# Kernel optimization log

Hardware: AMD Instinct MI355X
Metric: run time of the kernel (lower is better)

The kernel has to match this reference:

```python
import jax, jax.numpy as jnp
import numpy as np

N = 100000
E = 1600000
IN_F = 128
OUT_F = 32
HEADS = 6
NEG_SLOPE = 0.2


def setup_inputs() -> dict:
    key = jax.random.key(0)
    k1, k2, k3, k4, k5 = jax.random.split(key, 5)
    x = jax.random.normal(k1, (N, IN_F), dtype=jnp.float32)
    edge_index = jax.random.randint(k2, (2, E), 0, N, dtype=jnp.int64)
    # GATConv params (PyG layout): shared linear for src/dst, per-head attention vectors, bias
    glorot = lambda k, shape: jax.random.normal(k, shape, dtype=jnp.float32) * np.sqrt(2.0 / (shape[0] + shape[-1]))
    W = glorot(k3, (IN_F, HEADS * OUT_F))          # lin.weight^T
    att_src = glorot(k4, (HEADS, OUT_F)) * 0.1     # [H, C]
    att_dst = glorot(k5, (HEADS, OUT_F)) * 0.1
    bias = jnp.zeros((OUT_F,), dtype=jnp.float32)  # concat=False -> bias of size out_feature
    return {"x": x, "edge_index": edge_index, "W": W,
            "att_src": att_src, "att_dst": att_dst, "bias": bias}


def reference(x, edge_index, W, att_src, att_dst, bias):
    src, dst = edge_index[0], edge_index[1]
    # Linear projection to per-head features: [N, H, C]
    xp = (x @ W).reshape(N, HEADS, OUT_F)
    # Per-node attention logit halves: [N, H]
    a_s = jnp.einsum("nhc,hc->nh", xp, att_src)
    a_d = jnp.einsum("nhc,hc->nh", xp, att_dst)
    # Per-edge logits with LeakyReLU: [E, H]
    e = jax.nn.leaky_relu(a_s[src] + a_d[dst], negative_slope=NEG_SLOPE)
    # Segment softmax over edges grouped by destination node
    m = jax.ops.segment_max(e, dst, num_segments=N)            # [N, H]
    m = jnp.where(jnp.isfinite(m), m, 0.0)                     # empty segments -> -inf guard
    e = jnp.exp(e - m[dst])
    s = jax.ops.segment_sum(e, dst, num_segments=N)            # [N, H]
    alpha = e / (s[dst] + 1e-16)                               # [E, H]
    # Weighted scatter-add aggregation: [N, H, C]
    msg = xp[src] * alpha[:, :, None]
    out = jax.ops.segment_sum(msg, dst, num_segments=N)
    # concat=False -> mean over heads, add bias, then SELU
    out = out.mean(axis=1) + bias
    return jax.nn.selu(out)
```

## Files before the change

### kernel.cpp

```cpp
#include <hip/hip_runtime.h>


typedef __attribute__((ext_vector_type(8))) short short8;
typedef __attribute__((ext_vector_type(4))) float f32x4;

#define SK 136

__device__ __forceinline__ unsigned short f2bf(float f)
{
    unsigned int u = __float_as_uint(f);
    u = (u + 0x7fffu + ((u >> 16) & 1u)) >> 16;
    return (unsigned short)u;
}

__global__ __launch_bounds__(256) void k_prep(
    const float* __restrict__ W,
    const float* __restrict__ att_src, const float* __restrict__ att_dst,
    unsigned short* __restrict__ wat, unsigned short* __restrict__ Wb,
    int* __restrict__ deg, int N)
{
    int i = blockIdx.x * 256 + threadIdx.x;
    if (i < N) deg[i] = 0;
    if (i < 128 * 192) Wb[i] = f2bf(W[i]);
    if (i < 128 * 16) {
        int k = i >> 4, c = i & 15;
        float v = 0.f;
        if (c < 12) {
            int h = c < 6 ? c : c - 6;
            const float* av = (c < 6 ? att_src : att_dst) + h * 32;
            const float* wr = W + k * 192 + h * 32;
            #pragma unroll
            for (int j = 0; j < 32; ++j) v = fmaf(wr[j], av[j], v);
        }
        wat[i] = f2bf(v);
    }
}

__global__ __launch_bounds__(256) void k_gemm(
    const float* __restrict__ x, const unsigned short* __restrict__ Wb,
    const unsigned short* __restrict__ wat,
    unsigned short* __restrict__ xpb, float* __restrict__ a_s, float* __restrict__ a_d,
    int N)
{
    __shared__ __align__(16) unsigned short xt[64 * SK];
    const int t    = threadIdx.x;
    const int wave = t >> 6;
    const int lane = t & 63;
    const int ln   = lane & 15;
    const int q    = lane >> 4;
    const int n0   = blockIdx.x * 64;
    const int cb   = wave * 48;

    {
        const float4* x4 = (const float4*)x;
        #pragma unroll
        for (int it = 0; it < 8; ++it) {
            int i   = t + it * 256;
            int row = i >> 5;
            int c4  = i & 31;
            int gr  = n0 + row;
            if (gr > N - 1) gr = N - 1;
            float4 f = x4[(size_t)gr * 32 + c4];
            unsigned int u0 = (unsigned int)f2bf(f.x) | ((unsigned int)f2bf(f.y) << 16);
            unsigned int u1 = (unsigned int)f2bf(f.z) | ((unsigned int)f2bf(f.w) << 16);
            *(uint2*)(xt + row * SK + c4 * 4) = make_uint2(u0, u1);
        }
    }

    short8 bw[3][4];
    #pragma unroll
    for (int nt = 0; nt < 3; ++nt)
        #pragma unroll
        for (int kbi = 0; kbi < 4; ++kbi) {
            short8 v;
            #pragma unroll
            for (int j = 0; j < 8; ++j)
                v[j] = (short)Wb[(kbi * 32 + q * 8 + j) * 192 + cb + nt * 16 + ln];
            bw[nt][kbi] = v;
        }
    short8 bwa[4];
    #pragma unroll
    for (int kbi = 0; kbi < 4; ++kbi) {
        short8 v;
        #pragma unroll
        for (int j = 0; j < 8; ++j)
            v[j] = (short)wat[(kbi * 32 + q * 8 + j) * 16 + ln];
        bwa[kbi] = v;
    }

    __syncthreads();

    f32x4 acc[4][3];
    #pragma unroll
    for (int mt = 0; mt < 4; ++mt)
        #pragma unroll
        for (int nt = 0; nt < 3; ++nt) acc[mt][nt] = (f32x4)0.f;

    #pragma unroll
    for (int kbi = 0; kbi < 4; ++kbi) {
        #pragma unroll
        for (int mt = 0; mt < 4; ++mt) {
            short8 av = *(const short8*)(xt + (mt * 16 + ln) * SK + kbi * 32 + q * 8);
            #pragma unroll
            for (int nt = 0; nt < 3; ++nt)
                acc[mt][nt] = __builtin_amdgcn_mfma_f32_16x16x32_bf16(
                    av, bw[nt][kbi], acc[mt][nt], 0, 0, 0);
        }
    }

    f32x4 acca = (f32x4)0.f;
    #pragma unroll
    for (int kbi = 0; kbi < 4; ++kbi) {
        short8 av = *(const short8*)(xt + (wave * 16 + ln) * SK + kbi * 32 + q * 8);
        acca = __builtin_amdgcn_mfma_f32_16x16x32_bf16(av, bwa[kbi], acca, 0, 0, 0);
    }

    #pragma unroll
    for (int mt = 0; mt < 4; ++mt) {
        #pragma unroll
        for (int r = 0; r < 4; ++r) {
            int grow = n0 + mt * 16 + q * 4 + r;
            if (grow < N) {
                #pragma unroll
                for (int nt = 0; nt < 3; ++nt)
                    xpb[(size_t)grow * 192 + cb + nt * 16 + ln] = f2bf(acc[mt][nt][r]);
            }
        }
    }
    #pragma unroll
    for (int r = 0; r < 4; ++r) {
        int grow = n0 + wave * 16 + q * 4 + r;
        if (grow < N) {
            if (ln < 6)       a_s[(size_t)grow * 6 + ln]     = acca[r];
            else if (ln < 12) a_d[(size_t)grow * 6 + ln - 6] = acca[r];
        }
    }
}

__global__ void k_deg(const int* __restrict__ ei, int* __restrict__ deg,
                      int* __restrict__ rank, int E)
{
    int e = blockIdx.x * blockDim.x + threadIdx.x;
    if (e < E) rank[e] = atomicAdd(&deg[ei[E + e]], 1);
}

__global__ __launch_bounds__(256) void k_bsum(
    const int* __restrict__ deg, int* __restrict__ bsum, int N)
{
    __shared__ int sd[256];
    const int b = blockIdx.x, t = threadIdx.x;
    const int base = b * 1024;
    int s = 0;
    #pragma unroll
    for (int k = 0; k < 4; ++k) {
        int g = base + t + k * 256;
        if (g < N) s += deg[g];
    }
    sd[t] = s;
    __syncthreads();
    for (int o = 128; o; o >>= 1) {
        if (t < o) sd[t] += sd[t + o];
        __syncthreads();
    }
    if (t == 0) bsum[b] = sd[0];
}

__global__ __launch_bounds__(256) void k_off(
    const int* __restrict__ deg, const int* __restrict__ bsum,
    int* __restrict__ off, int N, int NB)
{
    __shared__ int sw[256];
    __shared__ int sbase;
    const int b = blockIdx.x, t = threadIdx.x;

    sw[t] = (t < b) ? bsum[t] : 0;
    __syncthreads();
    for (int o = 128; o; o >>= 1) {
        if (t < o) sw[t] += sw[t + o];
        __syncthreads();
    }
    if (t == 0) sbase = sw[0];
    __syncthreads();

    const int base = b * 1024 + t * 4;
    int d[4]; int s = 0;
    #pragma unroll
    for (int k = 0; k < 4; ++k) {
        int g = base + k;
        d[k] = (g < N) ? deg[g] : 0;
        s += d[k];
    }
    sw[t] = s;
    __syncthreads();
    for (int o = 1; o < 256; o <<= 1) {
        int add = (t >= o) ? sw[t - o] : 0;
        __syncthreads();
        sw[t] += add;
        __syncthreads();
    }
    int run = sbase + (sw[t] - s);
    #pragma unroll
    for (int k = 0; k < 4; ++k) {
        int g = base + k;
        if (g < N) off[g] = run;
        run += d[k];
    }
    if (b == NB - 1 && t == 255) off[N] = sbase + sw[255];
}

__global__ void k_scat(const int* __restrict__ ei, const int* __restrict__ off,
                       const int* __restrict__ rank, int* __restrict__ csr_src, int E)
{
    int e = blockIdx.x * blockDim.x + threadIdx.x;
    if (e < E) {
        int dst = ei[E + e];
        csr_src[off[dst] + rank[e]] = ei[e];
    }
}

__global__ __launch_bounds__(256) void k_agg(
    const unsigned short* __restrict__ xpb,
    const float* __restrict__ a_s, const float* __restrict__ a_d,
    const int* __restrict__ csr_src, const int* __restrict__ off,
    const float* __restrict__ bias, float* __restrict__ out, int N)
{
    const int wid = threadIdx.x >> 6;
    const int l   = threadIdx.x & 63;
    const int n = blockIdx.x * 4 + wid;
    if (n >= N) return;

    const int nb  = off[n];
    const int deg = off[n + 1] - nb;
    const int hr  = l >> 3;
    const int h   = hr < 6 ? hr : 5;
    const int lc  = l < 48 ? l : 47;
    const unsigned lcb = (unsigned)lc * 8u;
    const unsigned h4  = (unsigned)h * 4u;
    const char* __restrict__ xpB = (const char*)xpb;
    const char* __restrict__ asB = (const char*)a_s;

    const float zd = a_d[(size_t)n * 6 + h];

    float ax = 0.f, ay = 0.f, az = 0.f, aw = 0.f, se = 0.f;

    if (deg <= 64) {
        int my3 = (l < deg) ? csr_src[nb + l] * 3 : 0;
        int i = 0;
        for (; i + 8 <= deg; i += 8) {
            unsigned s3[8]; float as[8]; uint2 xv[8];
            #pragma unroll
            for (int k = 0; k < 8; ++k) {
                s3[k] = (unsigned)__shfl(my3, i + k);
                as[k] = *(const float*)(asB + s3[k] * 8u + h4);
            }
            #pragma unroll
            for (int k = 0; k < 8; ++k)
                xv[k] = *(const uint2*)(xpB + s3[k] * 128u + lcb);
            #pragma unroll
            for (int k = 0; k < 8; ++k) {
                float z = as[k] + zd;
                z = z > 0.f ? z : 0.2f * z;
                float ev = __expf(z);
                ax = fmaf(ev, __uint_as_float(xv[k].x << 16), ax);
                ay = fmaf(ev, __uint_as_float(xv[k].x & 0xffff0000u), ay);
                az = fmaf(ev, __uint_as_float(xv[k].y << 16), az);
                aw = fmaf(ev, __uint_as_float(xv[k].y & 0xffff0000u), aw);
                se += ev;
            }
        }
        for (; i < deg; ++i) {
            unsigned s3 = (unsigned)__shfl(my3, i);
            float z  = *(const float*)(asB + s3 * 8u + h4) + zd;
            z = z > 0.f ? z : 0.2f * z;
            float ev = __expf(z);
            uint2 xv = *(const uint2*)(xpB + s3 * 128u + lcb);
            ax = fmaf(ev, __uint_as_float(xv.x << 16), ax);
            ay = fmaf(ev, __uint_as_float(xv.x & 0xffff0000u), ay);
            az = fmaf(ev, __uint_as_float(xv.y << 16), az);
            aw = fmaf(ev, __uint_as_float(xv.y & 0xffff0000u), aw);
            se += ev;
        }
    } else {
        int i = 0;
        for (; i + 4 <= deg; i += 4) {
            unsigned s3[4]; float as[4]; uint2 xv[4];
            #pragma unroll
            for (int k = 0; k < 4; ++k) {
                s3[k] = (unsigned)csr_src[nb + i + k] * 3u;
                as[k] = *(const float*)(asB + s3[k] * 8u + h4);
            }
            #pragma unroll
            for (int k = 0; k < 4; ++k)
                xv[k] = *(const uint2*)(xpB + s3[k] * 128u + lcb);
            #pragma unroll
            for (int k = 0; k < 4; ++k) {
                float z = as[k] + zd;
                z = z > 0.f ? z : 0.2f * z;
                float ev = __expf(z);
                ax = fmaf(ev, __uint_as_float(xv[k].x << 16), ax);
                ay = fmaf(ev, __uint_as_float(xv[k].x & 0xffff0000u), ay);
                az = fmaf(ev, __uint_as_float(xv[k].y << 16), az);
                aw = fmaf(ev, __uint_as_float(xv[k].y & 0xffff0000u), aw);
                se += ev;
            }
        }
        for (; i < deg; ++i) {
            unsigned s3 = (unsigned)csr_src[nb + i] * 3u;
            float z  = *(const float*)(asB + s3 * 8u + h4) + zd;
            z = z > 0.f ? z : 0.2f * z;
            float ev = __expf(z);
            uint2 xv = *(const uint2*)(xpB + s3 * 128u + lcb);
            ax = fmaf(ev, __uint_as_float(xv.x << 16), ax);
            ay = fmaf(ev, __uint_as_float(xv.x & 0xffff0000u), ay);
            az = fmaf(ev, __uint_as_float(xv.y << 16), az);
            aw = fmaf(ev, __uint_as_float(xv.y & 0xffff0000u), aw);
            se += ev;
        }
    }

    const float inv = 1.f / (se + 1e-16f);
    float v0 = (l < 48) ? ax * inv : 0.f;
    float v1 = (l < 48) ? ay * inv : 0.f;
    float v2 = (l < 48) ? az * inv : 0.f;
    float v3 = (l < 48) ? aw * inv : 0.f;

    #pragma unroll
    for (int d = 8; d <= 32; d <<= 1) {
        v0 += __shfl_down(v0, d);
        v1 += __shfl_down(v1, d);
        v2 += __shfl_down(v2, d);
        v3 += __shfl_down(v3, d);
    }

    if (l < 8) {
        float4 b4 = ((const float4*)bias)[l];
        const float sc = 1.0507009873554805f, al = 1.6732632423543772f;
        float m[4] = {v0 * (1.f / 6.f) + b4.x, v1 * (1.f / 6.f) + b4.y,
                      v2 * (1.f / 6.f) + b4.z, v3 * (1.f / 6.f) + b4.w};
        #pragma unroll
        for (int k = 0; k < 4; ++k)
            m[k] = m[k] > 0.f ? sc * m[k] : sc * al * (__expf(m[k]) - 1.f);
        ((float4*)out)[(size_t)n * 8 + l] = make_float4(m[0], m[1], m[2], m[3]);
    }
}

extern "C" void kernel_launch(void* const* d_in, const int* in_sizes, int n_in,
                              void* d_out, int out_size, void* d_ws, size_t ws_size,
                              hipStream_t stream)
{
    const float* x       = (const float*)d_in[0];
    const int*   ei      = (const int*)d_in[1];
    const float* W       = (const float*)d_in[2];
    const float* att_src = (const float*)d_in[3];
    const float* att_dst = (const float*)d_in[4];
    const float* bias    = (const float*)d_in[5];
    float* out = (float*)d_out;

    const int N = in_sizes[0] / 128;
    const int E = in_sizes[1] / 2;
    const int NB = (N + 1023) / 1024;

    char* ws = (char*)d_ws;
    size_t o = 0;
    auto take = [&](size_t bytes) { size_t r = o; o = (o + bytes + 255) & ~(size_t)255; return r; };
    unsigned short* xpb = (unsigned short*)(ws + take((size_t)N * 192 * 2));
    float* a_s     = (float*)(ws + take((size_t)N * 6 * 4));
    float* a_d     = (float*)(ws + take((size_t)N * 6 * 4));
    int*   off     = (int*)  (ws + take((size_t)(N + 1) * 4));
    int*   deg     = (int*)  (ws + take((size_t)N * 4));
    int*   rank    = (int*)  (ws + take((size_t)E * 4));
    int*   csr_src = (int*)  (ws + take((size_t)E * 4));
    int*   bsum    = (int*)  (ws + take((size_t)NB * 4));
    unsigned short* wat = (unsigned short*)(ws + take((size_t)128 * 16 * 2));
    unsigned short* Wb  = (unsigned short*)(ws + take((size_t)128 * 192 * 2));
    (void)ws_size; (void)n_in; (void)out_size;

    int pg = (N + 255) / 256;
    k_prep<<<pg, 256, 0, stream>>>(W, att_src, att_dst, wat, Wb, deg, N);
    k_gemm<<<(N + 63) / 64, 256, 0, stream>>>(x, Wb, wat, xpb, a_s, a_d, N);
    int eg = (E + 255) / 256;
    k_deg<<<eg, 256, 0, stream>>>(ei, deg, rank, E);
    k_bsum<<<NB, 256, 0, stream>>>(deg, bsum, N);
    k_off<<<NB, 256, 0, stream>>>(deg, bsum, off, N, NB);
    k_scat<<<eg, 256, 0, stream>>>(ei, off, rank, csr_src, E);
    k_agg<<<(N + 3) / 4, 256, 0, stream>>>(xpb, a_s, a_d, csr_src, off, bias, out, N);
}
```

Before: 329.2 us.

## Fuse degree counting into GEMM launch and pack dst with rank

Merges the edge in-degree atomic counting into the projection GEMM kernel as extra blocks, so both run in one launch and can overlap. It also stores destination and rank in a single packed word, so the scatter kernel no longer rereads the destination row of the edge list. Packing assumes each node has fewer than 256 incoming edges and fewer than 2^24 nodes, which ties correctness to the degree distribution.

```diff
diff --git a/kernel.cpp b/kernel.cpp
--- a/kernel.cpp
+++ b/kernel.cpp
@@ -36,14 +36,27 @@
     }
 }
 
-__global__ __launch_bounds__(256) void k_gemm(
+__global__ __launch_bounds__(256) void k_gd(
     const float* __restrict__ x, const unsigned short* __restrict__ Wb,
     const unsigned short* __restrict__ wat,
     unsigned short* __restrict__ xpb, float* __restrict__ a_s, float* __restrict__ a_d,
-    int N)
+    const int* __restrict__ ei, int* __restrict__ deg, unsigned int* __restrict__ pack,
+    int N, int E, int GB, int DB)
 {
     __shared__ __align__(16) unsigned short xt[64 * SK];
-    const int t    = threadIdx.x;
+    const int t = threadIdx.x;
+
+    if ((int)blockIdx.x >= GB) {
+        const int bid = (int)blockIdx.x - GB;
+        const int stride = DB * 256;
+        for (int e = bid * 256 + t; e < E; e += stride) {
+            int dst = ei[E + e];
+            int r = atomicAdd(&deg[dst], 1);
+            pack[e] = ((unsigned int)dst << 8) | (unsigned int)r;
+        }
+        return;
+    }
+
     const int wave = t >> 6;
     const int lane = t & 63;
     const int ln   = lane & 15;
@@ -137,13 +150,6 @@
     }
 }
 
-__global__ void k_deg(const int* __restrict__ ei, int* __restrict__ deg,
-                      int* __restrict__ rank, int E)
-{
-    int e = blockIdx.x * blockDim.x + threadIdx.x;
-    if (e < E) rank[e] = atomicAdd(&deg[ei[E + e]], 1);
-}
-
 __global__ __launch_bounds__(256) void k_bsum(
     const int* __restrict__ deg, int* __restrict__ bsum, int N)
 {
@@ -209,12 +215,13 @@
 }
 
 __global__ void k_scat(const int* __restrict__ ei, const int* __restrict__ off,
-                       const int* __restrict__ rank, int* __restrict__ csr_src, int E)
+                       const unsigned int* __restrict__ pack,
+                       int* __restrict__ csr_src, int E)
 {
     int e = blockIdx.x * blockDim.x + threadIdx.x;
     if (e < E) {
-        int dst = ei[E + e];
-        csr_src[off[dst] + rank[e]] = ei[e];
+        unsigned int p = pack[e];
+        csr_src[off[p >> 8] + (int)(p & 255u)] = ei[e];
     }
 }
 
@@ -359,6 +366,8 @@
     const int N = in_sizes[0] / 128;
     const int E = in_sizes[1] / 2;
     const int NB = (N + 1023) / 1024;
+    const int GB = (N + 63) / 64;
+    const int DB = 1024;
 
     char* ws = (char*)d_ws;
     size_t o = 0;
@@ -368,7 +377,7 @@
     float* a_d     = (float*)(ws + take((size_t)N * 6 * 4));
     int*   off     = (int*)  (ws + take((size_t)(N + 1) * 4));
     int*   deg     = (int*)  (ws + take((size_t)N * 4));
-    int*   rank    = (int*)  (ws + take((size_t)E * 4));
+    unsigned int* pack = (unsigned int*)(ws + take((size_t)E * 4));
     int*   csr_src = (int*)  (ws + take((size_t)E * 4));
     int*   bsum    = (int*)  (ws + take((size_t)NB * 4));
     unsigned short* wat = (unsigned short*)(ws + take((size_t)128 * 16 * 2));
@@ -377,11 +386,11 @@
 
     int pg = (N + 255) / 256;
     k_prep<<<pg, 256, 0, stream>>>(W, att_src, att_dst, wat, Wb, deg, N);
-    k_gemm<<<(N + 63) / 64, 256, 0, stream>>>(x, Wb, wat, xpb, a_s, a_d, N);
-    int eg = (E + 255) / 256;
-    k_deg<<<eg, 256, 0, stream>>>(ei, deg, rank, E);
+    k_gd<<<GB + DB, 256, 0, stream>>>(x, Wb, wat, xpb, a_s, a_d,
+                                      ei, deg, pack, N, E, GB, DB);
     k_bsum<<<NB, 256, 0, stream>>>(deg, bsum, N);
     k_off<<<NB, 256, 0, stream>>>(deg, bsum, off, N, NB);
-    k_scat<<<eg, 256, 0, stream>>>(ei, off, rank, csr_src, E);
+    int eg = (E + 255) / 256;
+    k_scat<<<eg, 256, 0, stream>>>(ei, off, pack, csr_src, E);
     k_agg<<<(N + 3) / 4, 256, 0, stream>>>(xpb, a_s, a_d, csr_src, off, bias, out, N);
 }
```

After: 325.3 us. Within noise of the previous version (-1.2%).
